# Kernel optimization log

Hardware: AMD Instinct MI355X
Metric: run time of the kernel (lower is better)

Reference implementation:

```python
import jax, jax.numpy as jnp
import numpy as np

N_NODES = 20000
N_EDGES = 100000
N_SNAP = 2
N_DIM, E_DIM, OUT_DIM, HEADS = 64, 32, 64, 2


def edge_gat(x, ef, src, dst, Wn, We, al, ar, ae, b):
    # DGL EdgeGATConv: fc (no bias), edge-aware attention, edge softmax over
    # incoming edges, message = (ft_src + ft_edge) * alpha, final additive bias.
    H, D = al.shape
    ft = (x @ Wn).reshape(-1, H, D)                # [N,H,D]
    fe = (ef @ We).reshape(-1, H, D)               # [E,H,D]
    el = jnp.einsum('nhd,hd->nh', ft, al)          # [N,H]
    er = jnp.einsum('nhd,hd->nh', ft, ar)          # [N,H]
    ee = jnp.einsum('ehd,hd->eh', fe, ae)          # [E,H]
    logits = jax.nn.leaky_relu(el[src] + er[dst] + ee, 0.2)  # [E,H]
    m = jax.ops.segment_max(logits, dst, num_segments=N_NODES)
    p = jnp.exp(logits - m[dst])
    s = jax.ops.segment_sum(p, dst, num_segments=N_NODES)
    a = p / s[dst]                                 # edge softmax per dst node
    msg = (ft[src] + fe) * a[..., None]            # [E,H,D]
    return jax.ops.segment_sum(msg, dst, num_segments=N_NODES) + b  # [N,H,D]


def gnn_rnn(x, ef, src, dst, params):
    # GNN_RNN.forward per snapshot: stacked EdgeGAT layers, head-mean each.
    for (Wn, We, al, ar, ae, b) in params:
        x = edge_gat(x, ef, src, dst, Wn, We, al, ar, ae, b).mean(axis=1)
    return x


def _mk_layer(key, in_d, e_d, out_d, heads, scale=0.1):
    ks = jax.random.split(key, 6)
    return dict(
        Wn=jax.random.normal(ks[0], (in_d, heads * out_d), jnp.float32) * scale,
        We=jax.random.normal(ks[1], (e_d, heads * out_d), jnp.float32) * scale,
        al=jax.random.normal(ks[2], (heads, out_d), jnp.float32) * scale,
        ar=jax.random.normal(ks[3], (heads, out_d), jnp.float32) * scale,
        ae=jax.random.normal(ks[4], (heads, out_d), jnp.float32) * scale,
        b=jax.random.normal(ks[5], (heads, out_d), jnp.float32) * scale,
    )


def setup_inputs() -> dict:
    key = jax.random.key(0)
    ks = jax.random.split(key, 10)
    inp = {
        'x': jax.random.normal(ks[0], (N_SNAP, N_NODES, N_DIM), jnp.float32),
        'e': jax.random.normal(ks[1], (N_SNAP, N_EDGES, E_DIM), jnp.float32),
        'src': jax.random.randint(ks[2], (N_SNAP, N_EDGES), 0, N_NODES),
        'dst': jax.random.randint(ks[3], (N_SNAP, N_EDGES), 0, N_NODES),
    }
    enc0 = _mk_layer(ks[4], N_DIM, E_DIM, OUT_DIM, HEADS)
    enc1 = _mk_layer(ks[5], OUT_DIM, E_DIM, OUT_DIM, HEADS)
    dec0 = _mk_layer(ks[6], OUT_DIM, E_DIM, N_DIM, HEADS)
    dec1 = _mk_layer(ks[7], N_DIM, E_DIM, N_DIM, HEADS)
    for pref, lp in [('enc0', enc0), ('enc1', enc1), ('dec0', dec0), ('dec1', dec1)]:
        for k, v in lp.items():
            inp[f'{pref}_{k}'] = v
    inp['W_e2d'] = jax.random.normal(ks[8], (OUT_DIM, OUT_DIM), jnp.float32) * 0.1
    return inp


def reference(x, e, src, dst,
              enc0_Wn, enc0_We, enc0_al, enc0_ar, enc0_ae, enc0_b,
              enc1_Wn, enc1_We, enc1_al, enc1_ar, enc1_ae, enc1_b,
              W_e2d,
              dec0_Wn, dec0_We, dec0_al, dec0_ar, dec0_ae, dec0_b,
              dec1_Wn, dec1_We, dec1_al, dec1_ar, dec1_ae, dec1_b):
    enc_params = [(enc0_Wn, enc0_We, enc0_al, enc0_ar, enc0_ae, enc0_b),
                  (enc1_Wn, enc1_We, enc1_al, enc1_ar, enc1_ae, enc1_b)]
    dec_params = [(dec0_Wn, dec0_We, dec0_al, dec0_ar, dec0_ae, dec0_b),
                  (dec1_Wn, dec1_We, dec1_al, dec1_ar, dec1_ae, dec1_b)]

    def per_snapshot(xs, es, ss, ds):
        h = gnn_rnn(xs, es, ss, ds, enc_params)   # encoder, [N,out_dim]
        h = h @ W_e2d.T                           # encoder_to_decoder (no bias)
        return gnn_rnn(h, es, ss, ds, dec_params) # decoder, [N,n_dim]

    decoded = jax.vmap(per_snapshot)(x, e, src, dst)  # [S,N,n_dim]
    return decoded[-1]
```

## Files before the change

### kernel.cpp

```cpp
#include <hip/hip_runtime.h>
#include <math.h>

#define N_NODES 20000
#define N_EDGES 100000

__device__ __forceinline__ float rl_f(float v, int l) {
    return __uint_as_float(__builtin_amdgcn_readlane(__float_as_uint(v), l));
}
__device__ __forceinline__ int rl_i(int v, int l) {
    return __builtin_amdgcn_readlane(v, l);
}
__device__ __forceinline__ float lrelu(float x) { return x > 0.f ? x : 0.2f * x; }

__global__ __launch_bounds__(256) void scan_kernel(const int* __restrict__ cnt,
                                                   int* __restrict__ row_ptr) {
    __shared__ int sdata[256];
    __shared__ int swsum[4];
    const int tid = threadIdx.x;
    const int b = blockIdx.x;
    int idx = b * 256 + tid;
    int v = (idx < N_NODES) ? cnt[idx] : 0;
    sdata[tid] = v;
    int partial = 0;
    for (int i = tid; i < b * 256; i += 256) partial += cnt[i];
#pragma unroll
    for (int off = 32; off; off >>= 1) partial += __shfl_xor(partial, off);
    if ((tid & 63) == 0) swsum[tid >> 6] = partial;
    __syncthreads();
    const int boff = swsum[0] + swsum[1] + swsum[2] + swsum[3];
    for (int off = 1; off < 256; off <<= 1) {
        int t_ = (tid >= off) ? sdata[tid - off] : 0;
        __syncthreads();
        sdata[tid] += t_;
        __syncthreads();
    }
    if (idx < N_NODES) row_ptr[idx] = boff + sdata[tid] - v;
    if (b == 0 && tid == 0) row_ptr[N_NODES] = N_EDGES;
}

__global__ __launch_bounds__(256) void setup_kernel(
    const int* __restrict__ dst, int* __restrict__ cnt, int* __restrict__ pos,
    const float* __restrict__ Wn0, const float* __restrict__ al0, const float* __restrict__ ar0,
    const float* __restrict__ Wn1, const float* __restrict__ al1, const float* __restrict__ ar1,
    const float* __restrict__ dWn, const float* __restrict__ al2, const float* __restrict__ ar2,
    const float* __restrict__ Wn3, const float* __restrict__ al3, const float* __restrict__ ar3,
    const float* __restrict__ W_e2d,
    const float* __restrict__ We0, const float* __restrict__ ae0,
    const float* __restrict__ We1, const float* __restrict__ ae1,
    const float* __restrict__ We2, const float* __restrict__ ae2,
    const float* __restrict__ We3, const float* __restrict__ ae3,
    const float* __restrict__ X0,
    float* __restrict__ P4, float* __restrict__ Q, float4* __restrict__ Wpack,
    float2* __restrict__ EL2, float2* __restrict__ ER2) {
    __shared__ float praw[256];
    const int t = threadIdx.x;
    const int bb = blockIdx.x;

    if (bb < 391) {
        int e = bb * 256 + t;
        if (e < N_EDGES) pos[e] = atomicAdd(&cnt[dst[e]], 1);
        return;
    }
    const int b = bb - 391;

    if (b < 4) {
        const int L = b;
        if (L != 2) {
            const float* Wn = (L == 0) ? Wn0 : (L == 1) ? Wn1 : Wn3;
            const float* al = (L == 0) ? al0 : (L == 1) ? al1 : al3;
            const float* ar = (L == 0) ? ar0 : (L == 1) ? ar1 : ar3;
            const int k = t >> 2, o = t & 3;
            const float* a = (o & 2) ? ar : al;
            const int h = o & 1;
            float acc = 0.f;
#pragma unroll 8
            for (int d = 0; d < 64; d++) acc = fmaf(Wn[k * 128 + h * 64 + d], a[h * 64 + d], acc);
            P4[L * 256 + t] = acc;
        } else {
            {
                const int i = t >> 2, o = t & 3;
                const float* a = (o & 2) ? ar2 : al2;
                const int h = o & 1;
                float acc = 0.f;
#pragma unroll 8
                for (int d = 0; d < 64; d++) acc = fmaf(dWn[i * 128 + h * 64 + d], a[h * 64 + d], acc);
                praw[t] = acc;
            }
            __syncthreads();
            const int j = t >> 2, o = t & 3;
            float acc = 0.f;
#pragma unroll 8
            for (int i = 0; i < 64; i++) acc = fmaf(W_e2d[i * 64 + j], praw[i * 4 + o], acc);
            P4[2 * 256 + t] = acc;
        }
    } else if (b == 4) {
        const int k = t >> 3, o = t & 7, L = o >> 1, h = o & 1;
        const float* We = (L == 0) ? We0 : (L == 1) ? We1 : (L == 2) ? We2 : We3;
        const float* ae = (L == 0) ? ae0 : (L == 1) ? ae1 : (L == 2) ? ae2 : ae3;
        float acc = 0.f;
#pragma unroll 8
        for (int d = 0; d < 64; d++) acc = fmaf(We[k * 128 + h * 64 + d], ae[h * 64 + d], acc);
        Q[t] = acc;
    } else if (b < 53) {
        const int idx = (b - 5) * 256 + t;
        const int L = idx / 3072;
        const int sub = idx - L * 3072;
        if (sub < 2048) {
            const int k2 = sub >> 6, l = sub & 63;
            if (L != 2) {
                const float* Wn = (L == 0) ? Wn0 : (L == 1) ? Wn1 : Wn3;
                Wpack[idx] = make_float4(Wn[(2 * k2) * 128 + l], Wn[(2 * k2) * 128 + 64 + l],
                                         Wn[(2 * k2 + 1) * 128 + l], Wn[(2 * k2 + 1) * 128 + 64 + l]);
            } else {
                float a0 = 0.f, a1 = 0.f, a2 = 0.f, a3 = 0.f;
#pragma unroll 4
                for (int i = 0; i < 64; i++) {
                    float wa = W_e2d[i * 64 + 2 * k2], wb = W_e2d[i * 64 + 2 * k2 + 1];
                    float da = dWn[i * 128 + l], db = dWn[i * 128 + 64 + l];
                    a0 = fmaf(wa, da, a0);
                    a1 = fmaf(wa, db, a1);
                    a2 = fmaf(wb, da, a2);
                    a3 = fmaf(wb, db, a3);
                }
                Wpack[idx] = make_float4(a0, a1, a2, a3);
            }
        } else {
            const int s2 = sub - 2048;
            const int k2 = s2 >> 6, l = s2 & 63;
            const float* We = (L == 0) ? We0 : (L == 1) ? We1 : (L == 2) ? We2 : We3;
            Wpack[idx] = make_float4(We[(2 * k2) * 128 + l], We[(2 * k2) * 128 + 64 + l],
                                     We[(2 * k2 + 1) * 128 + l], We[(2 * k2 + 1) * 128 + 64 + l]);
        }
    } else {
        {
            const int k = t >> 2, o = t & 3;
            const float* a = (o & 2) ? ar0 : al0;
            const int h = o & 1;
            float acc = 0.f;
#pragma unroll 8
            for (int d = 0; d < 64; d++) acc = fmaf(Wn0[k * 128 + h * 64 + d], a[h * 64 + d], acc);
            praw[t] = acc;
        }
        __syncthreads();
        const int lane = t & 63;
        const int wave = t >> 6;
        const float px = praw[lane * 4 + 0], py = praw[lane * 4 + 1];
        const float pz = praw[lane * 4 + 2], pw = praw[lane * 4 + 3];
        const int nb = (int)gridDim.x - 444;
        for (int node = (b - 53) * 4 + wave; node < N_NODES; node += nb * 4) {
            float xv = X0[node * 64 + lane];
            float e0 = xv * px, e1 = xv * py, f0 = xv * pz, f1 = xv * pw;
#pragma unroll
            for (int off = 32; off; off >>= 1) {
                e0 += __shfl_xor(e0, off);
                e1 += __shfl_xor(e1, off);
                f0 += __shfl_xor(f0, off);
                f1 += __shfl_xor(f1, off);
            }
            if (lane == 0) {
                EL2[node] = make_float2(e0, e1);
                ER2[node] = make_float2(f0, f1);
            }
        }
    }
}

__global__ __launch_bounds__(256) void prep_kernel(const float* __restrict__ Efeat,
                                                   const int* __restrict__ src,
                                                   const int* __restrict__ dst,
                                                   const int* __restrict__ pos,
                                                   const int* __restrict__ row_ptr,
                                                   const float* __restrict__ Q,
                                                   float* __restrict__ E_csr,
                                                   int* __restrict__ src_csr,
                                                   float* __restrict__ EE_csr) {
    __shared__ float QS[256];
    __shared__ float ES[32][33];
    __shared__ int JS[32];
    const int tid = threadIdx.x;
    QS[tid] = Q[tid];
    const int e0 = blockIdx.x * 32;
    const int el_ = tid >> 3, quad = tid & 7;
    float4 v = ((const float4*)Efeat)[(size_t)(e0 + el_) * 8 + quad];
    ES[el_][quad * 4 + 0] = v.x;
    ES[el_][quad * 4 + 1] = v.y;
    ES[el_][quad * 4 + 2] = v.z;
    ES[el_][quad * 4 + 3] = v.w;
    if (tid < 32) {
        int e = e0 + tid;
        int j = row_ptr[dst[e]] + pos[e];
        JS[tid] = j;
        src_csr[j] = src[e];
    }
    __syncthreads();
    const int j = JS[el_];
    ((float4*)E_csr)[(size_t)j * 8 + quad] = v;
    const int o = quad;
    float acc = 0.f;
#pragma unroll
    for (int k = 0; k < 32; k++) acc = fmaf(ES[el_][k], QS[k * 8 + o], acc);
    EE_csr[(size_t)(o >> 1) * 2 * N_EDGES + (size_t)j * 2 + (o & 1)] = acc;
}

__global__ __launch_bounds__(256) void layer_kernel(
    const float* __restrict__ X,
    const float2* __restrict__ ELi, const float2* __restrict__ ERi,
    const float* __restrict__ E_csr, const int* __restrict__ src_csr,
    const int* __restrict__ row_ptr, const float2* __restrict__ EE_L,
    const float4* __restrict__ Wp, const float* __restrict__ bias,
    const float* __restrict__ P4next, const int has_next,
    float* __restrict__ OUT,
    float2* __restrict__ ELo, float2* __restrict__ ERo) {
    __shared__ float4 WS[2048];
    const int tid = threadIdx.x;
#pragma unroll
    for (int i = 0; i < 8; i++) WS[i * 256 + tid] = Wp[i * 256 + tid];
    const float4* __restrict__ WeG = Wp + 2048;

    const int lane = tid & 63;
    const int wave = tid >> 6;
    const int half = lane >> 5, hl = lane & 31;
    const int node = blockIdx.x * 4 + wave;
    const float bb0 = bias[lane], bb1 = bias[64 + lane];
    const float4 p = has_next ? ((const float4*)P4next)[lane] : make_float4(0.f, 0.f, 0.f, 0.f);
    __syncthreads();

    if (node >= N_NODES) return;
    {
        const int beg = row_ptr[node], end = row_ptr[node + 1];
        const int deg = end - beg;
        float ax0 = 0.f, ax1 = 0.f, aeh = 0.f;
        if (deg > 0) {
            const float2 er = ERi[node];
            float l0 = 0.f, l1 = 0.f, aX0 = 0.f, aX1 = 0.f, aE = 0.f;
            if (deg <= 64) {
                int sn = 0;
                float w0 = 0.f, w1 = 0.f;
                if (lane < deg) {
                    sn = src_csr[beg + lane];
                    float2 ee = EE_L[beg + lane];
                    float2 el = ELi[sn];
                    w0 = __expf(lrelu(el.x + er.x + ee.x));
                    w1 = __expf(lrelu(el.y + er.y + ee.y));
                }
                l0 = w0;
                l1 = w1;
#pragma unroll
                for (int off = 32; off; off >>= 1) {
                    l0 += __shfl_xor(l0, off);
                    l1 += __shfl_xor(l1, off);
                }
                const int dm1 = deg - 1;
                {
                    float xs[8], es[8];
#pragma unroll
                    for (int t = 0; t < 8; t++) {
                        int ct = t < dm1 ? t : dm1;
                        int st = rl_i(sn, ct);
                        xs[t] = X[st * 64 + lane];
                        es[t] = E_csr[(size_t)(beg + ct) * 32 + hl];
                    }
#pragma unroll
                    for (int t = 0; t < 8; t++) {
                        float w0t = rl_f(w0, t);
                        float w1t = rl_f(w1, t);
                        aX0 = fmaf(w0t, xs[t], aX0);
                        aX1 = fmaf(w1t, xs[t], aX1);
                        aE = fmaf(half ? w1t : w0t, es[t], aE);
                    }
                }
                int t = 8;
                for (; t + 4 <= deg; t += 4) {
                    int s0 = rl_i(sn, t), s1 = rl_i(sn, t + 1);
                    int s2 = rl_i(sn, t + 2), s3 = rl_i(sn, t + 3);
                    float x0 = X[s0 * 64 + lane];
                    float x1 = X[s1 * 64 + lane];
                    float x2 = X[s2 * 64 + lane];
                    float x3 = X[s3 * 64 + lane];
                    const float* Eb = E_csr + (size_t)(beg + t) * 32 + hl;
                    float e0 = Eb[0], e1 = Eb[32], e2 = Eb[64], e3 = Eb[96];
                    float w00 = rl_f(w0, t), w01 = rl_f(w0, t + 1);
                    float w02 = rl_f(w0, t + 2), w03 = rl_f(w0, t + 3);
                    float w10 = rl_f(w1, t), w11 = rl_f(w1, t + 1);
                    float w12 = rl_f(w1, t + 2), w13 = rl_f(w1, t + 3);
                    aX0 = fmaf(w00, x0, aX0); aX1 = fmaf(w10, x0, aX1);
                    aX0 = fmaf(w01, x1, aX0); aX1 = fmaf(w11, x1, aX1);
                    aX0 = fmaf(w02, x2, aX0); aX1 = fmaf(w12, x2, aX1);
                    aX0 = fmaf(w03, x3, aX0); aX1 = fmaf(w13, x3, aX1);
                    aE = fmaf(half ? w10 : w00, e0, aE);
                    aE = fmaf(half ? w11 : w01, e1, aE);
                    aE = fmaf(half ? w12 : w02, e2, aE);
                    aE = fmaf(half ? w13 : w03, e3, aE);
                }
                for (; t < deg; t++) {
                    int st = rl_i(sn, t);
                    float w0t = rl_f(w0, t), w1t = rl_f(w1, t);
                    float xv = X[st * 64 + lane];
                    float ev = E_csr[(size_t)(beg + t) * 32 + hl];
                    aX0 = fmaf(w0t, xv, aX0);
                    aX1 = fmaf(w1t, xv, aX1);
                    aE = fmaf(half ? w1t : w0t, ev, aE);
                }
            } else {
                for (int c = beg; c < end; c += 64) {
                    int jj = c + lane;
                    int sn_ = 0;
                    float w0c = 0.f, w1c = 0.f;
                    if (jj < end) {
                        sn_ = src_csr[jj];
                        float2 ee = EE_L[jj];
                        float2 el = ELi[sn_];
                        w0c = __expf(lrelu(el.x + er.x + ee.x));
                        w1c = __expf(lrelu(el.y + er.y + ee.y));
                    }
                    float s0_ = w0c, s1_ = w1c;
#pragma unroll
                    for (int off = 32; off; off >>= 1) {
                        s0_ += __shfl_xor(s0_, off);
                        s1_ += __shfl_xor(s1_, off);
                    }
                    l0 += s0_;
                    l1 += s1_;
                    int nch = (end - c) < 64 ? (end - c) : 64;
                    int t = 0;
                    for (; t + 4 <= nch; t += 4) {
                        int q0 = rl_i(sn_, t), q1 = rl_i(sn_, t + 1);
                        int q2 = rl_i(sn_, t + 2), q3 = rl_i(sn_, t + 3);
                        float x0 = X[q0 * 64 + lane];
                        float x1 = X[q1 * 64 + lane];
                        float x2 = X[q2 * 64 + lane];
                        float x3 = X[q3 * 64 + lane];
                        const float* Eb = E_csr + (size_t)(c + t) * 32 + hl;
                        float e0 = Eb[0], e1 = Eb[32], e2 = Eb[64], e3 = Eb[96];
                        float w00 = rl_f(w0c, t), w01 = rl_f(w0c, t + 1);
                        float w02 = rl_f(w0c, t + 2), w03 = rl_f(w0c, t + 3);
                        float w10 = rl_f(w1c, t), w11 = rl_f(w1c, t + 1);
                        float w12 = rl_f(w1c, t + 2), w13 = rl_f(w1c, t + 3);
                        aX0 = fmaf(w00, x0, aX0); aX1 = fmaf(w10, x0, aX1);
                        aX0 = fmaf(w01, x1, aX0); aX1 = fmaf(w11, x1, aX1);
                        aX0 = fmaf(w02, x2, aX0); aX1 = fmaf(w12, x2, aX1);
                        aX0 = fmaf(w03, x3, aX0); aX1 = fmaf(w13, x3, aX1);
                        aE = fmaf(half ? w10 : w00, e0, aE);
                        aE = fmaf(half ? w11 : w01, e1, aE);
                        aE = fmaf(half ? w12 : w02, e2, aE);
                        aE = fmaf(half ? w13 : w03, e3, aE);
                    }
                    for (; t < nch; t++) {
                        int st = rl_i(sn_, t);
                        float w0t = rl_f(w0c, t), w1t = rl_f(w1c, t);
                        float xv = X[st * 64 + lane];
                        float ev = E_csr[(size_t)(c + t) * 32 + hl];
                        aX0 = fmaf(w0t, xv, aX0);
                        aX1 = fmaf(w1t, xv, aX1);
                        aE = fmaf(half ? w1t : w0t, ev, aE);
                    }
                }
            }
            const float inv0 = l0 > 0.f ? 1.f / l0 : 0.f;
            const float inv1 = l1 > 0.f ? 1.f / l1 : 0.f;
            ax0 = aX0 * inv0;
            ax1 = aX1 * inv1;
            aeh = aE * (half ? inv1 : inv0);
        }
        float r0 = 0.f, r1 = 0.f;
#pragma unroll
        for (int k2 = 0; k2 < 32; k2++) {
            float4 w4 = WS[k2 * 64 + lane];
            r0 = fmaf(rl_f(ax0, 2 * k2), w4.x, r0);
            r1 = fmaf(rl_f(ax1, 2 * k2), w4.y, r1);
            r0 = fmaf(rl_f(ax0, 2 * k2 + 1), w4.z, r0);
            r1 = fmaf(rl_f(ax1, 2 * k2 + 1), w4.w, r1);
        }
#pragma unroll
        for (int k2 = 0; k2 < 16; k2++) {
            float4 w4 = WeG[k2 * 64 + lane];
            r0 = fmaf(rl_f(aeh, 2 * k2), w4.x, r0);
            r1 = fmaf(rl_f(aeh, 32 + 2 * k2), w4.y, r1);
            r0 = fmaf(rl_f(aeh, 2 * k2 + 1), w4.z, r0);
            r1 = fmaf(rl_f(aeh, 32 + 2 * k2 + 1), w4.w, r1);
        }
        const float outv = 0.5f * (r0 + bb0 + r1 + bb1);
        OUT[node * 64 + lane] = outv;
        if (has_next) {
            float e0 = outv * p.x, e1 = outv * p.y, f0 = outv * p.z, f1 = outv * p.w;
#pragma unroll
            for (int off = 32; off; off >>= 1) {
                e0 += __shfl_xor(e0, off);
                e1 += __shfl_xor(e1, off);
                f0 += __shfl_xor(f0, off);
                f1 += __shfl_xor(f1, off);
            }
            if (lane == 0) {
                ELo[node] = make_float2(e0, e1);
                ERo[node] = make_float2(f0, f1);
            }
        }
    }
}

extern "C" void kernel_launch(void* const* d_in, const int* in_sizes, int n_in,
                              void* d_out, int out_size, void* d_ws, size_t ws_size,
                              hipStream_t stream) {
    const float* x = (const float*)d_in[0];
    const float* e = (const float*)d_in[1];
    const int* src = (const int*)d_in[2];
    const int* dst = (const int*)d_in[3];

    const float* x1 = x + (size_t)1 * N_NODES * 64;
    const float* e1 = e + (size_t)1 * N_EDGES * 32;
    const int* src1 = src + N_EDGES;
    const int* dst1 = dst + N_EDGES;

    int we2d_idx, dec0_b, dec1_b;
    if (in_sizes[16] == 64 * 64 && in_sizes[17] == 64 * 128) {
        we2d_idx = 16; dec0_b = 17; dec1_b = 23;
    } else {
        dec0_b = 16; dec1_b = 22; we2d_idx = 28;
    }
    auto P = [&](int i) { return (const float*)d_in[i]; };

    char* ws = (char*)d_ws;
    int* cnt      = (int*)(ws + 0);
    int* row_ptr  = (int*)(ws + 80000);
    int* pos      = (int*)(ws + 160064);
    float* q      = (float*)(ws + 560576);
    int* src_csr  = (int*)(ws + 561600);
    float* e_csr  = (float*)(ws + 961600);
    float* ee_csr = (float*)(ws + 13761600);
    float* p4_all = (float*)(ws + 16961600);
    float* elA    = (float*)(ws + 16965696);
    float* erA    = (float*)(ws + 17125696);
    float* elB    = (float*)(ws + 17285696);
    float* erB    = (float*)(ws + 17445696);
    float* h0     = (float*)(ws + 17605696);
    float* h1     = (float*)(ws + 22725696);
    float4* wpack = (float4*)(ws + 27845696);

    hipMemsetAsync(cnt, 0, N_NODES * sizeof(int), stream);

    setup_kernel<<<903, 256, 0, stream>>>(
        dst1, cnt, pos,
        P(4), P(6), P(7),
        P(10), P(12), P(13),
        P(dec0_b + 0), P(dec0_b + 2), P(dec0_b + 3),
        P(dec1_b + 0), P(dec1_b + 2), P(dec1_b + 3),
        P(we2d_idx),
        P(5), P(8), P(11), P(14),
        P(dec0_b + 1), P(dec0_b + 4), P(dec1_b + 1), P(dec1_b + 4),
        x1,
        p4_all, q, wpack, (float2*)elA, (float2*)erA);

    const int SB = (N_NODES + 255) / 256;
    scan_kernel<<<SB, 256, 0, stream>>>(cnt, row_ptr);

    prep_kernel<<<N_EDGES / 32, 256, 0, stream>>>(e1, src1, dst1, pos, row_ptr, q,
                                                  e_csr, src_csr, ee_csr);

    const int NB_L = (N_NODES + 3) / 4;
    auto run = [&](const float* Xin, int L, const float* bias_,
                   const float* elI, const float* erI,
                   float* Out, float* elO, float* erO, int hn) {
        layer_kernel<<<NB_L, 256, 0, stream>>>(
            Xin, (const float2*)elI, (const float2*)erI,
            e_csr, src_csr, row_ptr,
            (const float2*)ee_csr + (size_t)L * N_EDGES,
            wpack + (size_t)L * 3072, bias_,
            p4_all + (L + 1) * 256, hn,
            Out, (float2*)elO, (float2*)erO);
    };

    run(x1, 0, P(9),           elA, erA, h0, elB, erB, 1);
    run(h0, 1, P(15),          elB, erB, h1, elA, erA, 1);
    run(h1, 2, P(dec0_b + 5),  elA, erA, h0, elB, erB, 1);
    run(h0, 3, P(dec1_b + 5),  elB, erB, (float*)d_out, elA, erA, 0);
}
```

Baseline: 301.7 us.

## Process two destination nodes per wave to raise memory-level parallelism and amortize weight staging

Each wave now handles two destination nodes, interleaving their first eight gathers and the projection readlane/FMA loops so more independent loads are in flight. Each block now covers eight nodes instead of four, which halves the number of blocks and so halves how often the per-block shared-memory weight load runs. Row pointer and ER loads are hoisted above the weight staging. The cost is higher register pressure and a fallback path for high-degree nodes; the new grid size assumes N_NODES divides by 8, and the later loops run sequentially per node.

```diff
diff --git a/kernel.cpp b/kernel.cpp
--- a/kernel.cpp
+++ b/kernel.cpp
@@ -202,6 +202,123 @@
     EE_csr[(size_t)(o >> 1) * 2 * N_EDGES + (size_t)j * 2 + (o & 1)] = acc;
 }
 
+__device__ __forceinline__ void gather_one(
+    int beg, int end, float2 er,
+    const float* __restrict__ X, const float* __restrict__ E_csr,
+    const int* __restrict__ src_csr, const float2* __restrict__ ELi,
+    const float2* __restrict__ EE_L,
+    int lane, int half, int hl,
+    float& ax0, float& ax1, float& aeh) {
+    ax0 = 0.f; ax1 = 0.f; aeh = 0.f;
+    const int deg = end - beg;
+    if (deg == 0) return;
+    float l0 = 0.f, l1 = 0.f, aX0 = 0.f, aX1 = 0.f, aE = 0.f;
+    if (deg <= 64) {
+        int sn = 0;
+        float w0 = 0.f, w1 = 0.f;
+        if (lane < deg) {
+            sn = src_csr[beg + lane];
+            float2 ee = EE_L[beg + lane];
+            float2 el = ELi[sn];
+            w0 = __expf(lrelu(el.x + er.x + ee.x));
+            w1 = __expf(lrelu(el.y + er.y + ee.y));
+        }
+        l0 = w0; l1 = w1;
+#pragma unroll
+        for (int off = 32; off; off >>= 1) {
+            l0 += __shfl_xor(l0, off);
+            l1 += __shfl_xor(l1, off);
+        }
+        const int dm1 = deg - 1;
+        {
+            float xs[8], es[8];
+#pragma unroll
+            for (int t = 0; t < 8; t++) {
+                int ct = t < dm1 ? t : dm1;
+                int st = rl_i(sn, ct);
+                xs[t] = X[st * 64 + lane];
+                es[t] = E_csr[(size_t)(beg + ct) * 32 + hl];
+            }
+#pragma unroll
+            for (int t = 0; t < 8; t++) {
+                float w0t = rl_f(w0, t);
+                float w1t = rl_f(w1, t);
+                aX0 = fmaf(w0t, xs[t], aX0);
+                aX1 = fmaf(w1t, xs[t], aX1);
+                aE = fmaf(half ? w1t : w0t, es[t], aE);
+            }
+        }
+        int t = 8;
+        for (; t + 4 <= deg; t += 4) {
+            int s0 = rl_i(sn, t), s1 = rl_i(sn, t + 1);
+            int s2 = rl_i(sn, t + 2), s3 = rl_i(sn, t + 3);
+            float x0 = X[s0 * 64 + lane];
+            float x1 = X[s1 * 64 + lane];
+            float x2 = X[s2 * 64 + lane];
+            float x3 = X[s3 * 64 + lane];
+            const float* Eb = E_csr + (size_t)(beg + t) * 32 + hl;
+            float e0 = Eb[0], e1 = Eb[32], e2 = Eb[64], e3 = Eb[96];
+            float w00 = rl_f(w0, t), w01 = rl_f(w0, t + 1);
+            float w02 = rl_f(w0, t + 2), w03 = rl_f(w0, t + 3);
+            float w10 = rl_f(w1, t), w11 = rl_f(w1, t + 1);
+            float w12 = rl_f(w1, t + 2), w13 = rl_f(w1, t + 3);
+            aX0 = fmaf(w00, x0, aX0); aX1 = fmaf(w10, x0, aX1);
+            aX0 = fmaf(w01, x1, aX0); aX1 = fmaf(w11, x1, aX1);
+            aX0 = fmaf(w02, x2, aX0); aX1 = fmaf(w12, x2, aX1);
+            aX0 = fmaf(w03, x3, aX0); aX1 = fmaf(w13, x3, aX1);
+            aE = fmaf(half ? w10 : w00, e0, aE);
+            aE = fmaf(half ? w11 : w01, e1, aE);
+            aE = fmaf(half ? w12 : w02, e2, aE);
+            aE = fmaf(half ? w13 : w03, e3, aE);
+        }
+        for (; t < deg; t++) {
+            int st = rl_i(sn, t);
+            float w0t = rl_f(w0, t), w1t = rl_f(w1, t);
+            float xv = X[st * 64 + lane];
+            float ev = E_csr[(size_t)(beg + t) * 32 + hl];
+            aX0 = fmaf(w0t, xv, aX0);
+            aX1 = fmaf(w1t, xv, aX1);
+            aE = fmaf(half ? w1t : w0t, ev, aE);
+        }
+    } else {
+        for (int c = beg; c < end; c += 64) {
+            int jj = c + lane;
+            int sn_ = 0;
+            float w0c = 0.f, w1c = 0.f;
+            if (jj < end) {
+                sn_ = src_csr[jj];
+                float2 ee = EE_L[jj];
+                float2 el = ELi[sn_];
+                w0c = __expf(lrelu(el.x + er.x + ee.x));
+                w1c = __expf(lrelu(el.y + er.y + ee.y));
+            }
+            float s0_ = w0c, s1_ = w1c;
+#pragma unroll
+            for (int off = 32; off; off >>= 1) {
+                s0_ += __shfl_xor(s0_, off);
+                s1_ += __shfl_xor(s1_, off);
+            }
+            l0 += s0_;
+            l1 += s1_;
+            int nch = (end - c) < 64 ? (end - c) : 64;
+            for (int t = 0; t < nch; t++) {
+                int st = rl_i(sn_, t);
+                float w0t = rl_f(w0c, t), w1t = rl_f(w1c, t);
+                float xv = X[st * 64 + lane];
+                float ev = E_csr[(size_t)(c + t) * 32 + hl];
+                aX0 = fmaf(w0t, xv, aX0);
+                aX1 = fmaf(w1t, xv, aX1);
+                aE = fmaf(half ? w1t : w0t, ev, aE);
+            }
+        }
+    }
+    const float inv0 = l0 > 0.f ? 1.f / l0 : 0.f;
+    const float inv1 = l1 > 0.f ? 1.f / l1 : 0.f;
+    ax0 = aX0 * inv0;
+    ax1 = aX1 * inv1;
+    aeh = aE * (half ? inv1 : inv0);
+}
+
 __global__ __launch_bounds__(256) void layer_kernel(
     const float* __restrict__ X,
     const float2* __restrict__ ELi, const float2* __restrict__ ERi,
@@ -213,187 +330,206 @@
     float2* __restrict__ ELo, float2* __restrict__ ERo) {
     __shared__ float4 WS[2048];
     const int tid = threadIdx.x;
-#pragma unroll
-    for (int i = 0; i < 8; i++) WS[i * 256 + tid] = Wp[i * 256 + tid];
-    const float4* __restrict__ WeG = Wp + 2048;
-
     const int lane = tid & 63;
     const int wave = tid >> 6;
     const int half = lane >> 5, hl = lane & 31;
-    const int node = blockIdx.x * 4 + wave;
+
+    const int n0 = blockIdx.x * 8 + wave * 2;
+    const int n1 = n0 + 1;
+    const int beg0 = row_ptr[n0];
+    const int beg1 = row_ptr[n1];
+    const int end1 = row_ptr[n1 + 1];
+    const float2 er0 = ERi[n0];
+    const float2 er1 = ERi[n1];
     const float bb0 = bias[lane], bb1 = bias[64 + lane];
     const float4 p = has_next ? ((const float4*)P4next)[lane] : make_float4(0.f, 0.f, 0.f, 0.f);
+
+#pragma unroll
+    for (int i = 0; i < 8; i++) WS[i * 256 + tid] = Wp[i * 256 + tid];
+    const float4* __restrict__ WeG = Wp + 2048;
     __syncthreads();
 
-    if (node >= N_NODES) return;
-    {
-        const int beg = row_ptr[node], end = row_ptr[node + 1];
-        const int deg = end - beg;
-        float ax0 = 0.f, ax1 = 0.f, aeh = 0.f;
-        if (deg > 0) {
-            const float2 er = ERi[node];
-            float l0 = 0.f, l1 = 0.f, aX0 = 0.f, aX1 = 0.f, aE = 0.f;
-            if (deg <= 64) {
-                int sn = 0;
-                float w0 = 0.f, w1 = 0.f;
-                if (lane < deg) {
-                    sn = src_csr[beg + lane];
-                    float2 ee = EE_L[beg + lane];
-                    float2 el = ELi[sn];
-                    w0 = __expf(lrelu(el.x + er.x + ee.x));
-                    w1 = __expf(lrelu(el.y + er.y + ee.y));
-                }
-                l0 = w0;
-                l1 = w1;
-#pragma unroll
-                for (int off = 32; off; off >>= 1) {
-                    l0 += __shfl_xor(l0, off);
-                    l1 += __shfl_xor(l1, off);
-                }
-                const int dm1 = deg - 1;
-                {
-                    float xs[8], es[8];
-#pragma unroll
-                    for (int t = 0; t < 8; t++) {
-                        int ct = t < dm1 ? t : dm1;
-                        int st = rl_i(sn, ct);
-                        xs[t] = X[st * 64 + lane];
-                        es[t] = E_csr[(size_t)(beg + ct) * 32 + hl];
-                    }
-#pragma unroll
-                    for (int t = 0; t < 8; t++) {
-                        float w0t = rl_f(w0, t);
-                        float w1t = rl_f(w1, t);
-                        aX0 = fmaf(w0t, xs[t], aX0);
-                        aX1 = fmaf(w1t, xs[t], aX1);
-                        aE = fmaf(half ? w1t : w0t, es[t], aE);
-                    }
-                }
-                int t = 8;
-                for (; t + 4 <= deg; t += 4) {
-                    int s0 = rl_i(sn, t), s1 = rl_i(sn, t + 1);
-                    int s2 = rl_i(sn, t + 2), s3 = rl_i(sn, t + 3);
-                    float x0 = X[s0 * 64 + lane];
-                    float x1 = X[s1 * 64 + lane];
-                    float x2 = X[s2 * 64 + lane];
-                    float x3 = X[s3 * 64 + lane];
-                    const float* Eb = E_csr + (size_t)(beg + t) * 32 + hl;
-                    float e0 = Eb[0], e1 = Eb[32], e2 = Eb[64], e3 = Eb[96];
-                    float w00 = rl_f(w0, t), w01 = rl_f(w0, t + 1);
-                    float w02 = rl_f(w0, t + 2), w03 = rl_f(w0, t + 3);
-                    float w10 = rl_f(w1, t), w11 = rl_f(w1, t + 1);
-                    float w12 = rl_f(w1, t + 2), w13 = rl_f(w1, t + 3);
-                    aX0 = fmaf(w00, x0, aX0); aX1 = fmaf(w10, x0, aX1);
-                    aX0 = fmaf(w01, x1, aX0); aX1 = fmaf(w11, x1, aX1);
-                    aX0 = fmaf(w02, x2, aX0); aX1 = fmaf(w12, x2, aX1);
-                    aX0 = fmaf(w03, x3, aX0); aX1 = fmaf(w13, x3, aX1);
-                    aE = fmaf(half ? w10 : w00, e0, aE);
-                    aE = fmaf(half ? w11 : w01, e1, aE);
-                    aE = fmaf(half ? w12 : w02, e2, aE);
-                    aE = fmaf(half ? w13 : w03, e3, aE);
-                }
-                for (; t < deg; t++) {
-                    int st = rl_i(sn, t);
-                    float w0t = rl_f(w0, t), w1t = rl_f(w1, t);
-                    float xv = X[st * 64 + lane];
-                    float ev = E_csr[(size_t)(beg + t) * 32 + hl];
-                    aX0 = fmaf(w0t, xv, aX0);
-                    aX1 = fmaf(w1t, xv, aX1);
-                    aE = fmaf(half ? w1t : w0t, ev, aE);
-                }
-            } else {
-                for (int c = beg; c < end; c += 64) {
-                    int jj = c + lane;
-                    int sn_ = 0;
-                    float w0c = 0.f, w1c = 0.f;
-                    if (jj < end) {
-                        sn_ = src_csr[jj];
-                        float2 ee = EE_L[jj];
-                        float2 el = ELi[sn_];
-                        w0c = __expf(lrelu(el.x + er.x + ee.x));
-                        w1c = __expf(lrelu(el.y + er.y + ee.y));
-                    }
-                    float s0_ = w0c, s1_ = w1c;
-#pragma unroll
-                    for (int off = 32; off; off >>= 1) {
-                        s0_ += __shfl_xor(s0_, off);
-                        s1_ += __shfl_xor(s1_, off);
-                    }
-                    l0 += s0_;
-                    l1 += s1_;
-                    int nch = (end - c) < 64 ? (end - c) : 64;
-                    int t = 0;
-                    for (; t + 4 <= nch; t += 4) {
-                        int q0 = rl_i(sn_, t), q1 = rl_i(sn_, t + 1);
-                        int q2 = rl_i(sn_, t + 2), q3 = rl_i(sn_, t + 3);
-                        float x0 = X[q0 * 64 + lane];
-                        float x1 = X[q1 * 64 + lane];
-                        float x2 = X[q2 * 64 + lane];
-                        float x3 = X[q3 * 64 + lane];
-                        const float* Eb = E_csr + (size_t)(c + t) * 32 + hl;
-                        float e0 = Eb[0], e1 = Eb[32], e2 = Eb[64], e3 = Eb[96];
-                        float w00 = rl_f(w0c, t), w01 = rl_f(w0c, t + 1);
-                        float w02 = rl_f(w0c, t + 2), w03 = rl_f(w0c, t + 3);
-                        float w10 = rl_f(w1c, t), w11 = rl_f(w1c, t + 1);
-                        float w12 = rl_f(w1c, t + 2), w13 = rl_f(w1c, t + 3);
-                        aX0 = fmaf(w00, x0, aX0); aX1 = fmaf(w10, x0, aX1);
-                        aX0 = fmaf(w01, x1, aX0); aX1 = fmaf(w11, x1, aX1);
-                        aX0 = fmaf(w02, x2, aX0); aX1 = fmaf(w12, x2, aX1);
-                        aX0 = fmaf(w03, x3, aX0); aX1 = fmaf(w13, x3, aX1);
-                        aE = fmaf(half ? w10 : w00, e0, aE);
-                        aE = fmaf(half ? w11 : w01, e1, aE);
-                        aE = fmaf(half ? w12 : w02, e2, aE);
-                        aE = fmaf(half ? w13 : w03, e3, aE);
-                    }
-                    for (; t < nch; t++) {
-                        int st = rl_i(sn_, t);
-                        float w0t = rl_f(w0c, t), w1t = rl_f(w1c, t);
-                        float xv = X[st * 64 + lane];
-                        float ev = E_csr[(size_t)(c + t) * 32 + hl];
-                        aX0 = fmaf(w0t, xv, aX0);
-                        aX1 = fmaf(w1t, xv, aX1);
-                        aE = fmaf(half ? w1t : w0t, ev, aE);
-                    }
-                }
-            }
-            const float inv0 = l0 > 0.f ? 1.f / l0 : 0.f;
-            const float inv1 = l1 > 0.f ? 1.f / l1 : 0.f;
-            ax0 = aX0 * inv0;
-            ax1 = aX1 * inv1;
-            aeh = aE * (half ? inv1 : inv0);
-        }
-        float r0 = 0.f, r1 = 0.f;
-#pragma unroll
-        for (int k2 = 0; k2 < 32; k2++) {
-            float4 w4 = WS[k2 * 64 + lane];
-            r0 = fmaf(rl_f(ax0, 2 * k2), w4.x, r0);
-            r1 = fmaf(rl_f(ax1, 2 * k2), w4.y, r1);
-            r0 = fmaf(rl_f(ax0, 2 * k2 + 1), w4.z, r0);
-            r1 = fmaf(rl_f(ax1, 2 * k2 + 1), w4.w, r1);
-        }
-#pragma unroll
-        for (int k2 = 0; k2 < 16; k2++) {
-            float4 w4 = WeG[k2 * 64 + lane];
-            r0 = fmaf(rl_f(aeh, 2 * k2), w4.x, r0);
-            r1 = fmaf(rl_f(aeh, 32 + 2 * k2), w4.y, r1);
-            r0 = fmaf(rl_f(aeh, 2 * k2 + 1), w4.z, r0);
-            r1 = fmaf(rl_f(aeh, 32 + 2 * k2 + 1), w4.w, r1);
-        }
-        const float outv = 0.5f * (r0 + bb0 + r1 + bb1);
-        OUT[node * 64 + lane] = outv;
-        if (has_next) {
-            float e0 = outv * p.x, e1 = outv * p.y, f0 = outv * p.z, f1 = outv * p.w;
-#pragma unroll
-            for (int off = 32; off; off >>= 1) {
-                e0 += __shfl_xor(e0, off);
-                e1 += __shfl_xor(e1, off);
-                f0 += __shfl_xor(f0, off);
-                f1 += __shfl_xor(f1, off);
-            }
-            if (lane == 0) {
-                ELo[node] = make_float2(e0, e1);
-                ERo[node] = make_float2(f0, f1);
-            }
+    const int end0 = beg1;
+    const int deg0 = end0 - beg0;
+    const int deg1 = end1 - beg1;
+
+    float ax0a = 0.f, ax1a = 0.f, aeha = 0.f;
+    float ax0b = 0.f, ax1b = 0.f, aehb = 0.f;
+
+    if (deg0 > 0 && deg0 <= 64 && deg1 > 0 && deg1 <= 64) {
+        int sn0 = 0, sn1 = 0;
+        float w0a = 0.f, w1a = 0.f, w0b = 0.f, w1b = 0.f;
+        if (lane < deg0) {
+            sn0 = src_csr[beg0 + lane];
+            float2 ee = EE_L[beg0 + lane];
+            float2 el = ELi[sn0];
+            w0a = __expf(lrelu(el.x + er0.x + ee.x));
+            w1a = __expf(lrelu(el.y + er0.y + ee.y));
+        }
+        if (lane < deg1) {
+            sn1 = src_csr[beg1 + lane];
+            float2 ee = EE_L[beg1 + lane];
+            float2 el = ELi[sn1];
+            w0b = __expf(lrelu(el.x + er1.x + ee.x));
+            w1b = __expf(lrelu(el.y + er1.y + ee.y));
+        }
+        float l0a = w0a, l1a = w1a, l0b = w0b, l1b = w1b;
+#pragma unroll
+        for (int off = 32; off; off >>= 1) {
+            l0a += __shfl_xor(l0a, off);
+            l1a += __shfl_xor(l1a, off);
+            l0b += __shfl_xor(l0b, off);
+            l1b += __shfl_xor(l1b, off);
+        }
+        float aX0a = 0.f, aX1a = 0.f, aEa = 0.f;
+        float aX0b = 0.f, aX1b = 0.f, aEb = 0.f;
+        const int dma = deg0 - 1, dmb = deg1 - 1;
+        {
+            float xs0[8], es0[8], xs1[8], es1[8];
+#pragma unroll
+            for (int t = 0; t < 8; t++) {
+                int c0 = t < dma ? t : dma;
+                int c1 = t < dmb ? t : dmb;
+                int s0 = rl_i(sn0, c0);
+                int s1 = rl_i(sn1, c1);
+                xs0[t] = X[s0 * 64 + lane];
+                es0[t] = E_csr[(size_t)(beg0 + c0) * 32 + hl];
+                xs1[t] = X[s1 * 64 + lane];
+                es1[t] = E_csr[(size_t)(beg1 + c1) * 32 + hl];
+            }
+#pragma unroll
+            for (int t = 0; t < 8; t++) {
+                float w0t = rl_f(w0a, t), w1t = rl_f(w1a, t);
+                float v0t = rl_f(w0b, t), v1t = rl_f(w1b, t);
+                aX0a = fmaf(w0t, xs0[t], aX0a);
+                aX1a = fmaf(w1t, xs0[t], aX1a);
+                aEa = fmaf(half ? w1t : w0t, es0[t], aEa);
+                aX0b = fmaf(v0t, xs1[t], aX0b);
+                aX1b = fmaf(v1t, xs1[t], aX1b);
+                aEb = fmaf(half ? v1t : v0t, es1[t], aEb);
+            }
+        }
+        int t = 8;
+        for (; t + 4 <= deg0; t += 4) {
+            int s0 = rl_i(sn0, t), s1 = rl_i(sn0, t + 1);
+            int s2 = rl_i(sn0, t + 2), s3 = rl_i(sn0, t + 3);
+            float x0 = X[s0 * 64 + lane];
+            float x1 = X[s1 * 64 + lane];
+            float x2 = X[s2 * 64 + lane];
+            float x3 = X[s3 * 64 + lane];
+            const float* Eb = E_csr + (size_t)(beg0 + t) * 32 + hl;
+            float e0 = Eb[0], e1 = Eb[32], e2 = Eb[64], e3 = Eb[96];
+            float w00 = rl_f(w0a, t), w01 = rl_f(w0a, t + 1);
+            float w02 = rl_f(w0a, t + 2), w03 = rl_f(w0a, t + 3);
+            float w10 = rl_f(w1a, t), w11 = rl_f(w1a, t + 1);
+            float w12 = rl_f(w1a, t + 2), w13 = rl_f(w1a, t + 3);
+            aX0a = fmaf(w00, x0, aX0a); aX1a = fmaf(w10, x0, aX1a);
+            aX0a = fmaf(w01, x1, aX0a); aX1a = fmaf(w11, x1, aX1a);
+            aX0a = fmaf(w02, x2, aX0a); aX1a = fmaf(w12, x2, aX1a);
+            aX0a = fmaf(w03, x3, aX0a); aX1a = fmaf(w13, x3, aX1a);
+            aEa = fmaf(half ? w10 : w00, e0, aEa);
+            aEa = fmaf(half ? w11 : w01, e1, aEa);
+            aEa = fmaf(half ? w12 : w02, e2, aEa);
+            aEa = fmaf(half ? w13 : w03, e3, aEa);
+        }
+        for (; t < deg0; t++) {
+            int st = rl_i(sn0, t);
+            float w0t = rl_f(w0a, t), w1t = rl_f(w1a, t);
+            float xv = X[st * 64 + lane];
+            float ev = E_csr[(size_t)(beg0 + t) * 32 + hl];
+            aX0a = fmaf(w0t, xv, aX0a);
+            aX1a = fmaf(w1t, xv, aX1a);
+            aEa = fmaf(half ? w1t : w0t, ev, aEa);
+        }
+        t = 8;
+        for (; t + 4 <= deg1; t += 4) {
+            int s0 = rl_i(sn1, t), s1 = rl_i(sn1, t + 1);
+            int s2 = rl_i(sn1, t + 2), s3 = rl_i(sn1, t + 3);
+            float x0 = X[s0 * 64 + lane];
+            float x1 = X[s1 * 64 + lane];
+            float x2 = X[s2 * 64 + lane];
+            float x3 = X[s3 * 64 + lane];
+            const float* Eb = E_csr + (size_t)(beg1 + t) * 32 + hl;
+            float e0 = Eb[0], e1 = Eb[32], e2 = Eb[64], e3 = Eb[96];
+            float w00 = rl_f(w0b, t), w01 = rl_f(w0b, t + 1);
+            float w02 = rl_f(w0b, t + 2), w03 = rl_f(w0b, t + 3);
+            float w10 = rl_f(w1b, t), w11 = rl_f(w1b, t + 1);
+            float w12 = rl_f(w1b, t + 2), w13 = rl_f(w1b, t + 3);
+            aX0b = fmaf(w00, x0, aX0b); aX1b = fmaf(w10, x0, aX1b);
+            aX0b = fmaf(w01, x1, aX0b); aX1b = fmaf(w11, x1, aX1b);
+            aX0b = fmaf(w02, x2, aX0b); aX1b = fmaf(w12, x2, aX1b);
+            aX0b = fmaf(w03, x3, aX0b); aX1b = fmaf(w13, x3, aX1b);
+            aEb = fmaf(half ? w10 : w00, e0, aEb);
+            aEb = fmaf(half ? w11 : w01, e1, aEb);
+            aEb = fmaf(half ? w12 : w02, e2, aEb);
+            aEb = fmaf(half ? w13 : w03, e3, aEb);
+        }
+        for (; t < deg1; t++) {
+            int st = rl_i(sn1, t);
+            float w0t = rl_f(w0b, t), w1t = rl_f(w1b, t);
+            float xv = X[st * 64 + lane];
+            float ev = E_csr[(size_t)(beg1 + t) * 32 + hl];
+            aX0b = fmaf(w0t, xv, aX0b);
+            aX1b = fmaf(w1t, xv, aX1b);
+            aEb = fmaf(half ? w1t : w0t, ev, aEb);
+        }
+        const float i0a = l0a > 0.f ? 1.f / l0a : 0.f;
+        const float i1a = l1a > 0.f ? 1.f / l1a : 0.f;
+        const float i0b = l0b > 0.f ? 1.f / l0b : 0.f;
+        const float i1b = l1b > 0.f ? 1.f / l1b : 0.f;
+        ax0a = aX0a * i0a; ax1a = aX1a * i1a; aeha = aEa * (half ? i1a : i0a);
+        ax0b = aX0b * i0b; ax1b = aX1b * i1b; aehb = aEb * (half ? i1b : i0b);
+    } else {
+        gather_one(beg0, end0, er0, X, E_csr, src_csr, ELi, EE_L, lane, half, hl,
+                   ax0a, ax1a, aeha);
+        gather_one(beg1, end1, er1, X, E_csr, src_csr, ELi, EE_L, lane, half, hl,
+                   ax0b, ax1b, aehb);
+    }
+
+    float r0a = 0.f, r1a = 0.f, r0b = 0.f, r1b = 0.f;
+#pragma unroll
+    for (int k2 = 0; k2 < 32; k2++) {
+        float4 w4 = WS[k2 * 64 + lane];
+        float a00 = rl_f(ax0a, 2 * k2), a01 = rl_f(ax0a, 2 * k2 + 1);
+        float a10 = rl_f(ax1a, 2 * k2), a11 = rl_f(ax1a, 2 * k2 + 1);
+        float c00 = rl_f(ax0b, 2 * k2), c01 = rl_f(ax0b, 2 * k2 + 1);
+        float c10 = rl_f(ax1b, 2 * k2), c11 = rl_f(ax1b, 2 * k2 + 1);
+        r0a = fmaf(a00, w4.x, r0a); r1a = fmaf(a10, w4.y, r1a);
+        r0a = fmaf(a01, w4.z, r0a); r1a = fmaf(a11, w4.w, r1a);
+        r0b = fmaf(c00, w4.x, r0b); r1b = fmaf(c10, w4.y, r1b);
+        r0b = fmaf(c01, w4.z, r0b); r1b = fmaf(c11, w4.w, r1b);
+    }
+#pragma unroll
+    for (int k2 = 0; k2 < 16; k2++) {
+        float4 w4 = WeG[k2 * 64 + lane];
+        float a00 = rl_f(aeha, 2 * k2), a01 = rl_f(aeha, 2 * k2 + 1);
+        float a10 = rl_f(aeha, 32 + 2 * k2), a11 = rl_f(aeha, 32 + 2 * k2 + 1);
+        float c00 = rl_f(aehb, 2 * k2), c01 = rl_f(aehb, 2 * k2 + 1);
+        float c10 = rl_f(aehb, 32 + 2 * k2), c11 = rl_f(aehb, 32 + 2 * k2 + 1);
+        r0a = fmaf(a00, w4.x, r0a); r1a = fmaf(a10, w4.y, r1a);
+        r0a = fmaf(a01, w4.z, r0a); r1a = fmaf(a11, w4.w, r1a);
+        r0b = fmaf(c00, w4.x, r0b); r1b = fmaf(c10, w4.y, r1b);
+        r0b = fmaf(c01, w4.z, r0b); r1b = fmaf(c11, w4.w, r1b);
+    }
+    const float outa = 0.5f * (r0a + bb0 + r1a + bb1);
+    const float outb = 0.5f * (r0b + bb0 + r1b + bb1);
+    OUT[n0 * 64 + lane] = outa;
+    OUT[n1 * 64 + lane] = outb;
+    if (has_next) {
+        float e0a = outa * p.x, e1a = outa * p.y, f0a = outa * p.z, f1a = outa * p.w;
+        float e0b = outb * p.x, e1b = outb * p.y, f0b = outb * p.z, f1b = outb * p.w;
+#pragma unroll
+        for (int off = 32; off; off >>= 1) {
+            e0a += __shfl_xor(e0a, off); e1a += __shfl_xor(e1a, off);
+            f0a += __shfl_xor(f0a, off); f1a += __shfl_xor(f1a, off);
+            e0b += __shfl_xor(e0b, off); e1b += __shfl_xor(e1b, off);
+            f0b += __shfl_xor(f0b, off); f1b += __shfl_xor(f1b, off);
+        }
+        if (lane == 0) {
+            ELo[n0] = make_float2(e0a, e1a);
+            ERo[n0] = make_float2(f0a, f1a);
+            ELo[n1] = make_float2(e0b, e1b);
+            ERo[n1] = make_float2(f0b, f1b);
         }
     }
 }
@@ -456,7 +592,7 @@
     prep_kernel<<<N_EDGES / 32, 256, 0, stream>>>(e1, src1, dst1, pos, row_ptr, q,
                                                   e_csr, src_csr, ee_csr);
 
-    const int NB_L = (N_NODES + 3) / 4;
+    const int NB_L = N_NODES / 8;
     auto run = [&](const float* Xin, int L, const float* bias_,
                    const float* elI, const float* erI,
                    float* Out, float* elO, float* erO, int hn) {
```

New measurement: 274.5 us. 1.1x faster.
